# Optimization experiments

Measured on AMD Instinct MI355X. Metric: run time of the kernel, lower is better.

Reference implementation:

```python
import jax, jax.numpy as jnp
import numpy as np

N, E, D_IN, D_OUT = 50000, 800000, 96, 256
BN_EPS = 1e-3  # Keras BatchNormalization default epsilon


def setup_inputs() -> dict:
    key = jax.random.key(0)
    ks = jax.random.split(key, 8)
    return {
        "x": jax.random.normal(ks[0], (N, D_IN), dtype=jnp.float32),
        "adj_src": jax.random.randint(ks[1], (E,), 0, N, dtype=jnp.int32),
        "adj_dst": jax.random.randint(ks[2], (E,), 0, N, dtype=jnp.int32),
        "adj_vals": jax.random.uniform(ks[3], (E,), dtype=jnp.float32),
        "eps": jax.random.normal(ks[4], (1,), dtype=jnp.float32) * 0.05,
        "W0": jax.random.normal(ks[5], (D_IN, D_OUT), dtype=jnp.float32) * 0.05,
        "W1": jax.random.normal(ks[6], (D_OUT, D_OUT), dtype=jnp.float32) * 0.05,
        "gamma": jnp.ones((D_OUT,), dtype=jnp.float32),
        "beta": jnp.zeros((D_OUT,), dtype=jnp.float32),
        "bn_mean": jnp.zeros((D_OUT,), dtype=jnp.float32),
        "bn_var": jnp.ones((D_OUT,), dtype=jnp.float32),
    }


def reference(x, adj_src, adj_dst, adj_vals, eps, W0, W1, gamma, beta, bn_mean, bn_var):
    n = x.shape[0]
    # Sparse adjacency SpMM: out[d] = sum_{e: dst(e)=d} vals[e] * x[src(e)]
    msgs = adj_vals[:, None] * x[adj_src]              # [E, D_IN]
    agg = jax.ops.segment_sum(msgs, adj_dst, num_segments=n)  # [N, D_IN]
    h = agg + eps * x                                   # eps residual (GIN)
    # MLP layer 0: matmul -> BN (inference) -> ReLU (dropout identity at eval)
    h = h @ W0                                           # [N, D_OUT]
    h = (h - bn_mean) * jax.lax.rsqrt(bn_var + BN_EPS) * gamma + beta
    h = jax.nn.relu(h)
    # Final matmul
    return h @ W1                                        # [N, D_OUT]
```

## Files before the change

kernel.cpp:

```cpp
#include <hip/hip_runtime.h>

#define D_IN   96
#define D_OUT  256
#define BN_EPS 1e-3f
#define TROWS  32
#define CAP    64
#define N_PAD  50048
#define RS1    104
#define RS2    264

typedef __attribute__((ext_vector_type(8))) short  short8;
typedef __attribute__((ext_vector_type(4))) float  floatx4;

__device__ __forceinline__ unsigned short f2bf(float f) {
    unsigned int u = __float_as_uint(f);
    unsigned int r = u + 0x7FFFu + ((u >> 16) & 1u);
    return (unsigned short)(r >> 16);
}
__device__ __forceinline__ float bfbits(unsigned short u) {
    return __uint_as_float(((unsigned int)u) << 16);
}

__global__ __launch_bounds__(256) void prep(
    const int* __restrict__ src, const int* __restrict__ dst,
    const float* __restrict__ vals, const float* __restrict__ x,
    const float* __restrict__ W0, const float* __restrict__ W1,
    int* __restrict__ cursor, int* __restrict__ bucket,
    unsigned short* __restrict__ xbf,
    unsigned short* __restrict__ W0p, unsigned short* __restrict__ W1p,
    int E, int n, int nscat, int nxc)
{
    const int b = blockIdx.x, tid = threadIdx.x;
    if (b < nscat) {
        int t = b * 256 + tid;
        if (t < E) {
            int d = dst[t];
            unsigned int u = __float_as_uint(vals[t]);
            unsigned int vhi = (u + 0x7FFFu + ((u >> 16) & 1u)) & 0xFFFF0000u;
            int pos = atomicAdd(&cursor[d], 1);
            if (pos < CAP)
                bucket[(d << 6) + pos] = (int)(vhi | (unsigned int)src[t]);
        }
    } else if (b < nscat + nxc) {
        int t = (b - nscat) * 256 + tid;
        if (t * 4 < n * D_IN) {
            float4 v = *(const float4*)(x + (size_t)t * 4);
            ushort4 o;
            o.x = f2bf(v.x); o.y = f2bf(v.y); o.z = f2bf(v.z); o.w = f2bf(v.w);
            *(ushort4*)(xbf + (size_t)t * 4) = o;
        }
    } else {
        int o = (b - nscat - nxc) * 256 + tid;
        const int n0 = 3 * 256 * 32;
        const int n1 = 8 * 256 * 32;
        if (o < n0) {
            int kk = o & 31, nn = (o >> 5) & 255, kb = o >> 13;
            W0p[o] = f2bf(W0[(size_t)(kb * 32 + kk) * 256 + nn]);
        } else if (o < n0 + n1) {
            int o2 = o - n0;
            int kk = o2 & 31, nn = (o2 >> 5) & 255, kb = o2 >> 13;
            W1p[o2] = f2bf(W1[(size_t)(kb * 32 + kk) * 256 + nn]);
        }
    }
}

template<bool BF16X>
__global__ __launch_bounds__(256) void gin_fused(
    const float* __restrict__ x, const unsigned short* __restrict__ xbf,
    const int* __restrict__ deg, const int* __restrict__ bucket,
    const float* __restrict__ epsp,
    const unsigned short* __restrict__ W0p, const unsigned short* __restrict__ W1p,
    const float* __restrict__ gamma, const float* __restrict__ beta,
    const float* __restrict__ bn_mean, const float* __restrict__ bn_var,
    float* __restrict__ out, int n)
{
    __shared__ __align__(16) unsigned short Abuf[TROWS][RS1];
    __shared__ __align__(16) unsigned short Hbuf[TROWS][RS2];
    __shared__ float bn_scale[D_OUT];
    __shared__ float bn_shift[D_OUT];

    const int tid = threadIdx.x;
    const int rowbase = blockIdx.x * TROWS;
    const float epsv = *epsp;

    {
        float sc = gamma[tid] * rsqrtf(bn_var[tid] + BN_EPS);
        bn_scale[tid] = sc;
        bn_shift[tid] = fmaf(-bn_mean[tid], sc, beta[tid]);
    }

    {
        const int j   = tid & 7;
        const int rl  = tid >> 3;
        const int row = rowbase + rl;
        float acc[12];
#pragma unroll
        for (int q = 0; q < 12; ++q) acc[q] = 0.f;

        if (row < n) {
            const int dg = min(deg[row], CAP);
            const int* ep = bucket + (row << 6);

#define EDGE_FMA(vv, A, B, C)                                              \
            { acc[0] = fmaf(vv, A.x, acc[0]); acc[1] = fmaf(vv, A.y, acc[1]);  \
              acc[2] = fmaf(vv, A.z, acc[2]); acc[3] = fmaf(vv, A.w, acc[3]);  \
              acc[4] = fmaf(vv, B.x, acc[4]); acc[5] = fmaf(vv, B.y, acc[5]);  \
              acc[6] = fmaf(vv, B.z, acc[6]); acc[7] = fmaf(vv, B.w, acc[7]);  \
              acc[8] = fmaf(vv, C.x, acc[8]); acc[9] = fmaf(vv, C.y, acc[9]);  \
              acc[10] = fmaf(vv, C.z, acc[10]); acc[11] = fmaf(vv, C.w, acc[11]); }

            int e = 0;
            if (BF16X) {
                for (; e + 2 <= dg; e += 2) {
                    int p0 = ep[e], p1 = ep[e + 1];
                    float v0 = __uint_as_float((unsigned int)p0 & 0xFFFF0000u);
                    float v1 = __uint_as_float((unsigned int)p1 & 0xFFFF0000u);
                    const unsigned short* r0 = xbf + (size_t)(p0 & 0xFFFF) * D_IN + j * 12;
                    const unsigned short* r1 = xbf + (size_t)(p1 & 0xFFFF) * D_IN + j * 12;
                    ushort4 a0 = *(const ushort4*)(r0), b0 = *(const ushort4*)(r0 + 4), c0 = *(const ushort4*)(r0 + 8);
                    ushort4 a1 = *(const ushort4*)(r1), b1 = *(const ushort4*)(r1 + 4), c1 = *(const ushort4*)(r1 + 8);
                    float4 A, B, C;
                    A.x = bfbits(a0.x); A.y = bfbits(a0.y); A.z = bfbits(a0.z); A.w = bfbits(a0.w);
                    B.x = bfbits(b0.x); B.y = bfbits(b0.y); B.z = bfbits(b0.z); B.w = bfbits(b0.w);
                    C.x = bfbits(c0.x); C.y = bfbits(c0.y); C.z = bfbits(c0.z); C.w = bfbits(c0.w);
                    EDGE_FMA(v0, A, B, C)
                    A.x = bfbits(a1.x); A.y = bfbits(a1.y); A.z = bfbits(a1.z); A.w = bfbits(a1.w);
                    B.x = bfbits(b1.x); B.y = bfbits(b1.y); B.z = bfbits(b1.z); B.w = bfbits(b1.w);
                    C.x = bfbits(c1.x); C.y = bfbits(c1.y); C.z = bfbits(c1.z); C.w = bfbits(c1.w);
                    EDGE_FMA(v1, A, B, C)
                }
                for (; e < dg; ++e) {
                    int p0 = ep[e];
                    float v0 = __uint_as_float((unsigned int)p0 & 0xFFFF0000u);
                    const unsigned short* r0 = xbf + (size_t)(p0 & 0xFFFF) * D_IN + j * 12;
                    ushort4 a0 = *(const ushort4*)(r0), b0 = *(const ushort4*)(r0 + 4), c0 = *(const ushort4*)(r0 + 8);
                    float4 A, B, C;
                    A.x = bfbits(a0.x); A.y = bfbits(a0.y); A.z = bfbits(a0.z); A.w = bfbits(a0.w);
                    B.x = bfbits(b0.x); B.y = bfbits(b0.y); B.z = bfbits(b0.z); B.w = bfbits(b0.w);
                    C.x = bfbits(c0.x); C.y = bfbits(c0.y); C.z = bfbits(c0.z); C.w = bfbits(c0.w);
                    EDGE_FMA(v0, A, B, C)
                }
                const unsigned short* rr = xbf + (size_t)row * D_IN + j * 12;
                ushort4 a0 = *(const ushort4*)(rr), b0 = *(const ushort4*)(rr + 4), c0 = *(const ushort4*)(rr + 8);
                float4 A, B, C;
                A.x = bfbits(a0.x); A.y = bfbits(a0.y); A.z = bfbits(a0.z); A.w = bfbits(a0.w);
                B.x = bfbits(b0.x); B.y = bfbits(b0.y); B.z = bfbits(b0.z); B.w = bfbits(b0.w);
                C.x = bfbits(c0.x); C.y = bfbits(c0.y); C.z = bfbits(c0.z); C.w = bfbits(c0.w);
                EDGE_FMA(epsv, A, B, C)
            } else {
                for (; e + 2 <= dg; e += 2) {
                    int p0 = ep[e], p1 = ep[e + 1];
                    float v0 = __uint_as_float((unsigned int)p0 & 0xFFFF0000u);
                    float v1 = __uint_as_float((unsigned int)p1 & 0xFFFF0000u);
                    const float* r0 = x + (size_t)(p0 & 0xFFFF) * D_IN + j * 12;
                    const float* r1 = x + (size_t)(p1 & 0xFFFF) * D_IN + j * 12;
                    float4 A0 = *(const float4*)(r0), B0 = *(const float4*)(r0 + 4), C0 = *(const float4*)(r0 + 8);
                    float4 A1 = *(const float4*)(r1), B1 = *(const float4*)(r1 + 4), C1 = *(const float4*)(r1 + 8);
                    EDGE_FMA(v0, A0, B0, C0)
                    EDGE_FMA(v1, A1, B1, C1)
                }
                for (; e < dg; ++e) {
                    int p0 = ep[e];
                    float v0 = __uint_as_float((unsigned int)p0 & 0xFFFF0000u);
                    const float* r0 = x + (size_t)(p0 & 0xFFFF) * D_IN + j * 12;
                    float4 A0 = *(const float4*)(r0), B0 = *(const float4*)(r0 + 4), C0 = *(const float4*)(r0 + 8);
                    EDGE_FMA(v0, A0, B0, C0)
                }
                const float* rr = x + (size_t)row * D_IN + j * 12;
                float4 A0 = *(const float4*)(rr), B0 = *(const float4*)(rr + 4), C0 = *(const float4*)(rr + 8);
                EDGE_FMA(epsv, A0, B0, C0)
            }
#undef EDGE_FMA
        }
#pragma unroll
        for (int q = 0; q < 6; ++q) {
            unsigned int lo = f2bf(acc[2 * q]);
            unsigned int hi = f2bf(acc[2 * q + 1]);
            *(unsigned int*)&Abuf[rl][j * 12 + 2 * q] = lo | (hi << 16);
        }
    }
    __syncthreads();

    const int lane = tid & 63;
    const int wid  = tid >> 6;
    const int quad = lane >> 4;
    const int nl   = lane & 15;

    floatx4 acc1[2][4];
#pragma unroll
    for (int mt = 0; mt < 2; ++mt)
#pragma unroll
        for (int nt = 0; nt < 4; ++nt)
            acc1[mt][nt] = (floatx4){0.f, 0.f, 0.f, 0.f};

#pragma unroll
    for (int kb = 0; kb < 3; ++kb) {
        short8 af0 = *(const short8*)&Abuf[nl     ][kb * 32 + quad * 8];
        short8 af1 = *(const short8*)&Abuf[16 + nl][kb * 32 + quad * 8];
#pragma unroll
        for (int nt = 0; nt < 4; ++nt) {
            const unsigned short* bp =
                W0p + ((size_t)(kb * 256 + wid * 64 + nt * 16 + nl)) * 32 + quad * 8;
            short8 bf = *(const short8*)bp;
            acc1[0][nt] = __builtin_amdgcn_mfma_f32_16x16x32_bf16(af0, bf, acc1[0][nt], 0, 0, 0);
            acc1[1][nt] = __builtin_amdgcn_mfma_f32_16x16x32_bf16(af1, bf, acc1[1][nt], 0, 0, 0);
        }
    }

#pragma unroll
    for (int mt = 0; mt < 2; ++mt)
#pragma unroll
        for (int nt = 0; nt < 4; ++nt) {
            int ncol = wid * 64 + nt * 16 + nl;
            float sc = bn_scale[ncol], sh = bn_shift[ncol];
#pragma unroll
            for (int r = 0; r < 4; ++r) {
                float h = fmaxf(0.f, fmaf(acc1[mt][nt][r], sc, sh));
                Hbuf[mt * 16 + quad * 4 + r][ncol] = f2bf(h);
            }
        }
    __syncthreads();

    floatx4 acc2[2][4];
#pragma unroll
    for (int mt = 0; mt < 2; ++mt)
#pragma unroll
        for (int nt = 0; nt < 4; ++nt)
            acc2[mt][nt] = (floatx4){0.f, 0.f, 0.f, 0.f};

#pragma unroll
    for (int kb = 0; kb < 8; ++kb) {
        short8 af0 = *(const short8*)&Hbuf[nl     ][kb * 32 + quad * 8];
        short8 af1 = *(const short8*)&Hbuf[16 + nl][kb * 32 + quad * 8];
#pragma unroll
        for (int nt = 0; nt < 4; ++nt) {
            const unsigned short* bp =
                W1p + ((size_t)(kb * 256 + wid * 64 + nt * 16 + nl)) * 32 + quad * 8;
            short8 bf = *(const short8*)bp;
            acc2[0][nt] = __builtin_amdgcn_mfma_f32_16x16x32_bf16(af0, bf, acc2[0][nt], 0, 0, 0);
            acc2[1][nt] = __builtin_amdgcn_mfma_f32_16x16x32_bf16(af1, bf, acc2[1][nt], 0, 0, 0);
        }
    }

#pragma unroll
    for (int mt = 0; mt < 2; ++mt)
#pragma unroll
        for (int nt = 0; nt < 4; ++nt) {
            int ncol = wid * 64 + nt * 16 + nl;
#pragma unroll
            for (int r = 0; r < 4; ++r) {
                int m = rowbase + mt * 16 + quad * 4 + r;
                if (m < n) out[(size_t)m * D_OUT + ncol] = acc2[mt][nt][r];
            }
        }
}

extern "C" void kernel_launch(void* const* d_in, const int* in_sizes, int n_in,
                              void* d_out, int out_size, void* d_ws, size_t ws_size,
                              hipStream_t stream) {
    const float* x       = (const float*)d_in[0];
    const int*   src     = (const int*)  d_in[1];
    const int*   dst     = (const int*)  d_in[2];
    const float* vals    = (const float*)d_in[3];
    const float* epsp    = (const float*)d_in[4];
    const float* W0      = (const float*)d_in[5];
    const float* W1      = (const float*)d_in[6];
    const float* gamma   = (const float*)d_in[7];
    const float* beta    = (const float*)d_in[8];
    const float* bn_mean = (const float*)d_in[9];
    const float* bn_var  = (const float*)d_in[10];
    float* out = (float*)d_out;

    const int n = in_sizes[0] / D_IN;
    const int E = in_sizes[1];

    int* cursor = (int*)d_ws;
    int* bucket = cursor + N_PAD;
    unsigned short* W0p = (unsigned short*)(bucket + (size_t)n * CAP);
    unsigned short* W1p = W0p + 3 * 256 * 32;
    unsigned short* xbf = W1p + 8 * 256 * 32;

    const size_t base_need = (size_t)(N_PAD + (size_t)n * CAP) * 4
                           + (size_t)(3 + 8) * 256 * 32 * 2;
    const bool use_bf16x = ws_size >= base_need + (size_t)n * D_IN * 2;

    hipMemsetAsync(cursor, 0, (size_t)n * sizeof(int), stream);

    const int nscat = (E + 255) / 256;
    const int nxc   = use_bf16x ? (n * D_IN / 4 + 255) / 256 : 0;
    const int nwc   = ((3 + 8) * 256 * 32 + 255) / 256;
    prep<<<nscat + nxc + nwc, 256, 0, stream>>>(
        src, dst, vals, x, W0, W1, cursor, bucket, xbf, W0p, W1p, E, n, nscat, nxc);

    const int gblocks = (n + TROWS - 1) / TROWS;
    if (use_bf16x)
        gin_fused<true><<<gblocks, 256, 0, stream>>>(
            x, xbf, cursor, bucket, epsp, W0p, W1p,
            gamma, beta, bn_mean, bn_var, out, n);
    else
        gin_fused<false><<<gblocks, 256, 0, stream>>>(
            x, xbf, cursor, bucket, epsp, W0p, W1p,
            gamma, beta, bn_mean, bn_var, out, n);
}
```

Measured before the change: 196.2 us.

## Vectorize prep scatter and conversion, alias shared buffers, add nontemporal loads/stores

The edge-scatter now handles four edges per thread with vector loads, and the x-to-bf16 conversion handles eight elements per thread. The fused kernel aliases Abuf and Hbuf in one shared array to cut LDS use, and adds a launch-bounds hint of 8 blocks to raise occupancy. A barrier is added before Hbuf is written so the aliased Abuf reads finish first. It also hoists the self-row load ahead of the edge loop and uses nontemporal loads for bucket entries and nontemporal stores for the output.

```diff
diff --git a/kernel.cpp b/kernel.cpp
--- a/kernel.cpp
+++ b/kernel.cpp
@@ -20,6 +20,14 @@
 __device__ __forceinline__ float bfbits(unsigned short u) {
     return __uint_as_float(((unsigned int)u) << 16);
 }
+
+#define SCAT(S, D, V) do {                                                  \
+    unsigned int u_ = __float_as_uint(V);                                   \
+    unsigned int vhi_ = (u_ + 0x7FFFu + ((u_ >> 16) & 1u)) & 0xFFFF0000u;   \
+    int pos_ = atomicAdd(&cursor[(D)], 1);                                  \
+    if (pos_ < CAP)                                                         \
+        bucket[((D) << 6) + pos_] = (int)(vhi_ | (unsigned int)(S));        \
+} while (0)
 
 __global__ __launch_bounds__(256) void prep(
     const int* __restrict__ src, const int* __restrict__ dst,
@@ -32,22 +40,32 @@
 {
     const int b = blockIdx.x, tid = threadIdx.x;
     if (b < nscat) {
-        int t = b * 256 + tid;
-        if (t < E) {
-            int d = dst[t];
-            unsigned int u = __float_as_uint(vals[t]);
-            unsigned int vhi = (u + 0x7FFFu + ((u >> 16) & 1u)) & 0xFFFF0000u;
-            int pos = atomicAdd(&cursor[d], 1);
-            if (pos < CAP)
-                bucket[(d << 6) + pos] = (int)(vhi | (unsigned int)src[t]);
+        int t = (b * 256 + tid) * 4;
+        if (t + 4 <= E) {
+            int4   s4 = *(const int4*)  (src  + t);
+            int4   d4 = *(const int4*)  (dst  + t);
+            float4 v4 = *(const float4*)(vals + t);
+            SCAT(s4.x, d4.x, v4.x);
+            SCAT(s4.y, d4.y, v4.y);
+            SCAT(s4.z, d4.z, v4.z);
+            SCAT(s4.w, d4.w, v4.w);
+        } else if (t < E) {
+            for (int q = t; q < E; ++q) {
+                int S = src[q], D = dst[q]; float V = vals[q];
+                SCAT(S, D, V);
+            }
         }
     } else if (b < nscat + nxc) {
-        int t = (b - nscat) * 256 + tid;
-        if (t * 4 < n * D_IN) {
-            float4 v = *(const float4*)(x + (size_t)t * 4);
-            ushort4 o;
-            o.x = f2bf(v.x); o.y = f2bf(v.y); o.z = f2bf(v.z); o.w = f2bf(v.w);
-            *(ushort4*)(xbf + (size_t)t * 4) = o;
+        size_t t   = (size_t)(b - nscat) * 256 + tid;
+        size_t off = t * 8;
+        if (off < (size_t)n * D_IN) {
+            float4 v0 = *(const float4*)(x + off);
+            float4 v1 = *(const float4*)(x + off + 4);
+            ushort4 o0, o1;
+            o0.x = f2bf(v0.x); o0.y = f2bf(v0.y); o0.z = f2bf(v0.z); o0.w = f2bf(v0.w);
+            o1.x = f2bf(v1.x); o1.y = f2bf(v1.y); o1.z = f2bf(v1.z); o1.w = f2bf(v1.w);
+            *(ushort4*)(xbf + off)     = o0;
+            *(ushort4*)(xbf + off + 4) = o1;
         }
     } else {
         int o = (b - nscat - nxc) * 256 + tid;
@@ -63,9 +81,10 @@
         }
     }
 }
+#undef SCAT
 
 template<bool BF16X>
-__global__ __launch_bounds__(256) void gin_fused(
+__global__ __launch_bounds__(256, 8) void gin_fused(
     const float* __restrict__ x, const unsigned short* __restrict__ xbf,
     const int* __restrict__ deg, const int* __restrict__ bucket,
     const float* __restrict__ epsp,
@@ -74,10 +93,11 @@
     const float* __restrict__ bn_mean, const float* __restrict__ bn_var,
     float* __restrict__ out, int n)
 {
-    __shared__ __align__(16) unsigned short Abuf[TROWS][RS1];
-    __shared__ __align__(16) unsigned short Hbuf[TROWS][RS2];
+    __shared__ __align__(16) unsigned short SMEM[TROWS * RS2];
     __shared__ float bn_scale[D_OUT];
     __shared__ float bn_shift[D_OUT];
+    unsigned short (*Abuf)[RS1] = (unsigned short (*)[RS1])SMEM;
+    unsigned short (*Hbuf)[RS2] = (unsigned short (*)[RS2])SMEM;
 
     const int tid = threadIdx.x;
     const int rowbase = blockIdx.x * TROWS;
@@ -111,8 +131,14 @@
 
             int e = 0;
             if (BF16X) {
+                const unsigned short* rr = xbf + (size_t)row * D_IN + j * 12;
+                ushort4 sa = *(const ushort4*)(rr);
+                ushort4 sb = *(const ushort4*)(rr + 4);
+                ushort4 sc = *(const ushort4*)(rr + 8);
+
                 for (; e + 2 <= dg; e += 2) {
-                    int p0 = ep[e], p1 = ep[e + 1];
+                    int p0 = __builtin_nontemporal_load(ep + e);
+                    int p1 = __builtin_nontemporal_load(ep + e + 1);
                     float v0 = __uint_as_float((unsigned int)p0 & 0xFFFF0000u);
                     float v1 = __uint_as_float((unsigned int)p1 & 0xFFFF0000u);
                     const unsigned short* r0 = xbf + (size_t)(p0 & 0xFFFF) * D_IN + j * 12;
@@ -130,7 +156,7 @@
                     EDGE_FMA(v1, A, B, C)
                 }
                 for (; e < dg; ++e) {
-                    int p0 = ep[e];
+                    int p0 = __builtin_nontemporal_load(ep + e);
                     float v0 = __uint_as_float((unsigned int)p0 & 0xFFFF0000u);
                     const unsigned short* r0 = xbf + (size_t)(p0 & 0xFFFF) * D_IN + j * 12;
                     ushort4 a0 = *(const ushort4*)(r0), b0 = *(const ushort4*)(r0 + 4), c0 = *(const ushort4*)(r0 + 8);
@@ -140,16 +166,17 @@
                     C.x = bfbits(c0.x); C.y = bfbits(c0.y); C.z = bfbits(c0.z); C.w = bfbits(c0.w);
                     EDGE_FMA(v0, A, B, C)
                 }
-                const unsigned short* rr = xbf + (size_t)row * D_IN + j * 12;
-                ushort4 a0 = *(const ushort4*)(rr), b0 = *(const ushort4*)(rr + 4), c0 = *(const ushort4*)(rr + 8);
-                float4 A, B, C;
-                A.x = bfbits(a0.x); A.y = bfbits(a0.y); A.z = bfbits(a0.z); A.w = bfbits(a0.w);
-                B.x = bfbits(b0.x); B.y = bfbits(b0.y); B.z = bfbits(b0.z); B.w = bfbits(b0.w);
-                C.x = bfbits(c0.x); C.y = bfbits(c0.y); C.z = bfbits(c0.z); C.w = bfbits(c0.w);
-                EDGE_FMA(epsv, A, B, C)
+                {
+                    float4 A, B, C;
+                    A.x = bfbits(sa.x); A.y = bfbits(sa.y); A.z = bfbits(sa.z); A.w = bfbits(sa.w);
+                    B.x = bfbits(sb.x); B.y = bfbits(sb.y); B.z = bfbits(sb.z); B.w = bfbits(sb.w);
+                    C.x = bfbits(sc.x); C.y = bfbits(sc.y); C.z = bfbits(sc.z); C.w = bfbits(sc.w);
+                    EDGE_FMA(epsv, A, B, C)
+                }
             } else {
                 for (; e + 2 <= dg; e += 2) {
-                    int p0 = ep[e], p1 = ep[e + 1];
+                    int p0 = __builtin_nontemporal_load(ep + e);
+                    int p1 = __builtin_nontemporal_load(ep + e + 1);
                     float v0 = __uint_as_float((unsigned int)p0 & 0xFFFF0000u);
                     float v1 = __uint_as_float((unsigned int)p1 & 0xFFFF0000u);
                     const float* r0 = x + (size_t)(p0 & 0xFFFF) * D_IN + j * 12;
@@ -160,7 +187,7 @@
                     EDGE_FMA(v1, A1, B1, C1)
                 }
                 for (; e < dg; ++e) {
-                    int p0 = ep[e];
+                    int p0 = __builtin_nontemporal_load(ep + e);
                     float v0 = __uint_as_float((unsigned int)p0 & 0xFFFF0000u);
                     const float* r0 = x + (size_t)(p0 & 0xFFFF) * D_IN + j * 12;
                     float4 A0 = *(const float4*)(r0), B0 = *(const float4*)(r0 + 4), C0 = *(const float4*)(r0 + 8);
@@ -206,6 +233,7 @@
             acc1[1][nt] = __builtin_amdgcn_mfma_f32_16x16x32_bf16(af1, bf, acc1[1][nt], 0, 0, 0);
         }
     }
+    __syncthreads();
 
 #pragma unroll
     for (int mt = 0; mt < 2; ++mt)
@@ -250,7 +278,9 @@
 #pragma unroll
             for (int r = 0; r < 4; ++r) {
                 int m = rowbase + mt * 16 + quad * 4 + r;
-                if (m < n) out[(size_t)m * D_OUT + ncol] = acc2[mt][nt][r];
+                if (m < n)
+                    __builtin_nontemporal_store(acc2[mt][nt][r],
+                                                out + (size_t)m * D_OUT + ncol);
             }
         }
 }
@@ -286,8 +316,8 @@
 
     hipMemsetAsync(cursor, 0, (size_t)n * sizeof(int), stream);
 
-    const int nscat = (E + 255) / 256;
-    const int nxc   = use_bf16x ? (n * D_IN / 4 + 255) / 256 : 0;
+    const int nscat = (E + 1023) / 1024;
+    const int nxc   = use_bf16x ? ((n * D_IN / 8) + 255) / 256 : 0;
     const int nwc   = ((3 + 8) * 256 * 32 + 255) / 256;
     prep<<<nscat + nxc + nwc, 256, 0, stream>>>(
         src, dst, vals, x, W0, W1, cursor, bucket, xbf, W0p, W1p, E, n, nscat, nxc);
```

New measurement: 225.6 us. 15.0% more time.
